# Optimization experiments

Hardware: AMD Instinct MI355X
Metric: run time of the kernel (lower is better)

## Reference

```python
import jax, jax.numpy as jnp
from jax import lax
import numpy as np

COST_CLASS, COST_BBOX, COST_GIOU = 2.0, 5.0, 2.0
ALPHA, GAMMA, OTA_K = 0.25, 2.0, 5
EXPANDED_STRIDES = 32.0
DEG = 180.0 / np.pi


def _make_corners(key, prefix):
    k1, k2, k3, k4, k5 = jax.random.split(key, 5)
    cx = jax.random.uniform(k1, prefix, minval=0.0, maxval=512.0)
    cy = jax.random.uniform(k2, prefix, minval=0.0, maxval=512.0)
    w = jax.random.uniform(k3, prefix, minval=8.0, maxval=128.0)
    h = jax.random.uniform(k4, prefix, minval=8.0, maxval=128.0)
    ang = jax.random.uniform(k5, prefix, minval=0.0, maxval=np.pi)
    offs = jnp.array([[-0.5, -0.5], [0.5, -0.5], [0.5, 0.5], [-0.5, 0.5]], jnp.float32)
    wh = jnp.stack([w, h], -1)[..., None, :]          # [..., 1, 2]
    pts = offs * wh                                    # [..., 4, 2]
    c, s = jnp.cos(ang)[..., None], jnp.sin(ang)[..., None]
    rx = pts[..., 0] * c - pts[..., 1] * s + cx[..., None]
    ry = pts[..., 0] * s + pts[..., 1] * c + cy[..., None]
    return jnp.stack([rx, ry], -1).reshape(prefix + (8,))


def setup_inputs() -> dict:
    key = jax.random.key(0)
    k1, k2, k3, k4 = jax.random.split(key, 4)
    B, Q, G, C = 16, 4096, 128, 80
    return {
        "pred_logits": jax.random.normal(k1, (B, Q, C), jnp.float32),
        "pred_boxes": _make_corners(k2, (B, Q)),
        "gt_boxes": _make_corners(k3, (B, G)),
        "gt_labels": jax.random.randint(k4, (B, G), 0, C),
    }


def corners_to_cxcywha(c):  # [N,8] -> [N,5]
    xc = (c[:, 0] + c[:, 2] + c[:, 4] + c[:, 6]) / 4
    yc = (c[:, 1] + c[:, 3] + c[:, 5] + c[:, 7]) / 4
    w = jnp.sqrt((c[:, 0] - c[:, 2]) ** 2 + (c[:, 1] - c[:, 3]) ** 2)
    h = jnp.sqrt((c[:, 2] - c[:, 4]) ** 2 + (c[:, 3] - c[:, 5]) ** 2)
    ang = jnp.arctan2(c[:, 3] - c[:, 1], c[:, 2] - c[:, 0]) * DEG
    return jnp.stack([xc, yc, w, h, ang], 1)


def _aabb(b5):
    cx, cy, w, h = b5[:, 0], b5[:, 1], b5[:, 2], b5[:, 3]
    return jnp.stack([cx - w / 2, cy - h / 2, cx + w / 2, cy + h / 2], 1)


def pairwise_iou(b1, b2):
    a, b = _aabb(b1), _aabb(b2)
    lt = jnp.maximum(a[:, None, :2], b[None, :, :2])
    rb = jnp.minimum(a[:, None, 2:], b[None, :, 2:])
    wh = jnp.clip(rb - lt, 0.0)
    inter = wh[..., 0] * wh[..., 1]
    area1 = (a[:, 2] - a[:, 0]) * (a[:, 3] - a[:, 1])
    area2 = (b[:, 2] - b[:, 0]) * (b[:, 3] - b[:, 1])
    return inter / (area1[:, None] + area2[None, :] - inter + 1e-8)


def pairwise_diou(b1, b2):
    iou = pairwise_iou(b1, b2)
    a, b = _aabb(b1), _aabb(b2)
    enc = jnp.maximum(a[:, None, 2:], b[None, :, 2:]) - jnp.minimum(a[:, None, :2], b[None, :, :2])
    c2 = (enc ** 2).sum(-1) + 1e-8
    d2 = ((b1[:, None, :2] - b2[None, :, :2]) ** 2).sum(-1)
    return iou - d2 / c2


def get_in_boxes_info(boxes, gts):
    bc = boxes.reshape(-1, 4, 2).mean(1)   # [Q,2]
    gp = gts.reshape(-1, 4, 2)             # [G,4,2]
    gc = gp.mean(1)                        # [G,2]
    cdist = jnp.sqrt(((bc[:, None] - gc[None]) ** 2).sum(-1))  # [Q,G]
    v1 = gp[:, 1] - gp[:, 0]
    v2 = gp[:, 2] - gp[:, 0]
    gt_area = jnp.abs(v1[:, 0] * v2[:, 1] - v1[:, 1] * v2[:, 0]) / 2
    diag = jnp.sqrt(((gp.max(1) - gp.min(1)) ** 2).sum(-1))
    radius = diag / EXPANDED_STRIDES
    in_boxes = cdist <= (gt_area / radius)[None, :]
    in_centers = cdist <= radius[None, :]
    return in_boxes.any(1), in_boxes & in_centers


def _dedup(cost, m):
    multi = m.sum(1) > 1
    onehot = jax.nn.one_hot(jnp.argmin(cost, 1), cost.shape[1], dtype=m.dtype)
    return jnp.where(multi[:, None], onehot, m)


def _match_single(logits, pboxes, gboxes, glabels):
    Q, G = pboxes.shape[0], gboxes.shape[0]
    prob = jax.nn.sigmoid(logits)
    fg_mask, _ = get_in_boxes_info(pboxes, gboxes)
    p5, g5 = corners_to_cxcywha(pboxes), corners_to_cxcywha(gboxes)
    ious = pairwise_iou(p5, g5)
    neg = (1 - ALPHA) * prob ** GAMMA * -jnp.log(1 - prob + 1e-8)
    pos = ALPHA * (1 - prob) ** GAMMA * -jnp.log(prob + 1e-8)
    cost_class = (pos - neg)[:, glabels]                         # [Q,G]
    cost_bbox = jnp.abs(pboxes[:, None] - gboxes[None]).sum(-1)  # L1 cdist on corners
    cost_giou = -pairwise_diou(p5, g5)
    # NB: source has `+ self.cost_giou * -cost_giou`, i.e. +w*diou; replicated verbatim.
    cost = COST_BBOX * cost_bbox + COST_CLASS * cost_class + COST_GIOU * (-cost_giou)
    cost = cost + 10000.0 * (~fg_mask)[:, None].astype(cost.dtype)
    # dynamic-k: sum of top OTA_K ious per gt, truncated to int, min 1
    topk = lax.top_k(ious.T, OTA_K)[0]                 # [G, k]
    dyn_k = jnp.clip(topk.sum(-1).astype(jnp.int32), 1, Q)
    ranks = jnp.argsort(jnp.argsort(cost, axis=0), axis=0)  # ascending-cost rank per column
    matching = (ranks < dyn_k[None, :]).astype(cost.dtype)
    matching = _dedup(cost, matching)
    # ensure every gt matched (bounded replication of the while loop)
    def cond(carry):
        c, m, it = carry
        return jnp.any(m.sum(0) == 0) & (it < G)
    def body(carry):
        c, m, it = carry
        c = c + 100000.0 * (m.sum(1) > 0)[:, None].astype(c.dtype)
        unm = m.sum(0) == 0
        amin = jnp.argmin(c, 0)                          # [G]
        hit = (jnp.arange(Q)[:, None] == amin[None, :]) & unm[None, :]
        m = jnp.where(hit, 1.0, m)
        m = _dedup(c, m)
        return (c, m, it + 1)
    _, matching, _ = lax.while_loop(cond, body, (cost, matching, jnp.int32(0)))
    return matching, cost, ious


def reference(pred_logits, pred_boxes, gt_boxes, gt_labels):
    return jax.vmap(_match_single)(pred_logits, pred_boxes, gt_boxes, gt_labels)
```

## Files before the change

### kernel.cpp

```cpp
#include <hip/hip_runtime.h>
#include <cstdint>
#include <cstddef>

#define B_ 16
#define Q_ 4096
#define G_ 128
#define C_ 80
#define QCHUNK 16
#define NCH (Q_ / QCHUNK)

typedef unsigned long long u64;
#define U64MAX 0xffffffffffffffffull

__device__ __forceinline__ u64 packkey(float v, int q) {
    unsigned int bts = __float_as_uint(v);
    if (bts == 0x80000000u) bts = 0u;
    bts = (bts & 0x80000000u) ? ~bts : (bts | 0x80000000u);
    return ((u64)bts << 32) | (unsigned int)q;
}

__device__ __forceinline__ u64 umin64(u64 a, u64 b) { return a < b ? a : b; }
__device__ __forceinline__ u64 umax64(u64 a, u64 b) { return a > b ? a : b; }

__device__ __forceinline__ void merge5_desc(
    float& a0, float& a1, float& a2, float& a3, float& a4,
    float b0, float b1, float b2, float b3, float b4)
{
    const float r0 = fmaxf(a0, b0);
    const float r1 = fmaxf(fmaxf(a1, b1), fminf(a0, b0));
    const float r2 = fmaxf(fmaxf(a2, b2), fmaxf(fminf(a0, b1), fminf(a1, b0)));
    const float r3 = fmaxf(fmaxf(a3, b3),
                     fmaxf(fminf(a0, b2), fmaxf(fminf(a1, b1), fminf(a2, b0))));
    const float r4 = fmaxf(fmaxf(a4, b4),
                     fmaxf(fmaxf(fminf(a0, b3), fminf(a3, b0)),
                           fmaxf(fminf(a1, b2), fminf(a2, b1))));
    a0 = r0; a1 = r1; a2 = r2; a3 = r3; a4 = r4;
}

__device__ __forceinline__ void merge5_asc(
    u64& a0, u64& a1, u64& a2, u64& a3, u64& a4,
    u64 b0, u64 b1, u64 b2, u64 b3, u64 b4)
{
    const u64 r0 = umin64(a0, b0);
    const u64 r1 = umin64(umin64(a1, b1), umax64(a0, b0));
    const u64 r2 = umin64(umin64(a2, b2), umin64(umax64(a0, b1), umax64(a1, b0)));
    const u64 r3 = umin64(umin64(a3, b3),
                   umin64(umax64(a0, b2), umin64(umax64(a1, b1), umax64(a2, b0))));
    const u64 r4 = umin64(umin64(a4, b4),
                   umin64(umin64(umax64(a0, b3), umax64(a3, b0)),
                          umin64(umax64(a1, b2), umax64(a2, b1))));
    a0 = r0; a1 = r1; a2 = r2; a3 = r3; a4 = r4;
}

__device__ __forceinline__ float focal_cost(float x) {
    float p;
    if (x >= 0.f) { const float e = expf(-x); p = 1.f / (1.f + e); }
    else          { const float e = expf(x);  p = e / (1.f + e); }
    const float pos = 0.25f * (1.f - p) * (1.f - p) * (-logf(p + 1e-8f));
    const float neg = 0.75f * p * p * (-logf(1.f - p + 1e-8f));
    return pos - neg;
}

__global__ __launch_bounds__(256) void fused_cost_kernel(
    const float* __restrict__ logits,
    const float* __restrict__ pboxes,
    const float* __restrict__ gboxes,
    const int*   __restrict__ glabels,
    float* __restrict__ out_cost,
    float* __restrict__ out_iou,
    float* __restrict__ costT,
    float* __restrict__ piou,
    u64*   __restrict__ pcost,
    int*   __restrict__ ramin)
{
    const int tid = threadIdx.x;
    const int g   = tid & 127;
    const int qh  = tid >> 7;
    const int ci  = blockIdx.x, b = blockIdx.y;
    const int q0  = ci * QCHUNK;

    __shared__ float pq[QCHUNK][16];
    __shared__ int   fgf[QCHUNK];
    __shared__ __align__(16) char lk_buf[5120];
    __shared__ float ctile[QCHUNK][G_ + 1];
    __shared__ float phalf[G_][5];
    float* lbuf = (float*)lk_buf;
    u64 (*khalf)[5] = (u64(*)[5])lk_buf;

    const float4* gb4 = (const float4*)(gboxes + ((size_t)b * G_ + g) * 8);
    const float4 gA = gb4[0], gB = gb4[1];
    const float g0 = gA.x, g1 = gA.y, g2 = gA.z, g3 = gA.w;
    const float g4 = gB.x, g5 = gB.y, g6 = gB.z, g7 = gB.w;
    const float gxc = (g0 + g2 + g4 + g6) * 0.25f;
    const float gyc = (g1 + g3 + g5 + g7) * 0.25f;
    const float gw = sqrtf((g0 - g2) * (g0 - g2) + (g1 - g3) * (g1 - g3));
    const float gh = sqrtf((g2 - g4) * (g2 - g4) + (g3 - g5) * (g3 - g5));
    const float gax0 = gxc - gw * 0.5f, gay0 = gyc - gh * 0.5f;
    const float gax1 = gxc + gw * 0.5f, gay1 = gyc + gh * 0.5f;
    const float garea = (gax1 - gax0) * (gay1 - gay0);
    const float v1x = g2 - g0, v1y = g3 - g1, v2x = g4 - g0, v2y = g5 - g1;
    const float gt_area = fabsf(v1x * v2y - v1y * v2x) * 0.5f;
    const float mxx = fmaxf(fmaxf(g0, g2), fmaxf(g4, g6));
    const float mnx = fminf(fminf(g0, g2), fminf(g4, g6));
    const float mxy = fmaxf(fmaxf(g1, g3), fmaxf(g5, g7));
    const float mny = fminf(fminf(g1, g3), fminf(g5, g7));
    const float dgx = mxx - mnx, dgy = mxy - mny;
    const float radius = sqrtf(dgx * dgx + dgy * dgy) / 32.0f;
    const float thresh = gt_area / radius;
    const int lab = glabels[b * G_ + g];

    if (tid < 32) {
        const float4 v = ((const float4*)(pboxes + ((size_t)b * Q_ + q0) * 8))[tid];
        *(float4*)&pq[tid >> 1][(tid & 1) * 4] = v;
    }
    __syncthreads();
    if (tid < QCHUNK) {
        const float* pr = pq[tid];
        const float p0 = pr[0], p1 = pr[1], p2 = pr[2], p3 = pr[3];
        const float p4 = pr[4], p5v = pr[5], p6 = pr[6], p7 = pr[7];
        const float pxc = (p0 + p2 + p4 + p6) * 0.25f;
        const float pyc = (p1 + p3 + p5v + p7) * 0.25f;
        const float pw = sqrtf((p0 - p2) * (p0 - p2) + (p1 - p3) * (p1 - p3));
        const float ph = sqrtf((p2 - p4) * (p2 - p4) + (p3 - p5v) * (p3 - p5v));
        pq[tid][8]  = pxc;
        pq[tid][9]  = pyc;
        pq[tid][10] = pxc - pw * 0.5f;
        pq[tid][11] = pyc - ph * 0.5f;
        pq[tid][12] = pxc + pw * 0.5f;
        pq[tid][13] = pyc + ph * 0.5f;
        pq[tid][14] = pw * ph;
        fgf[tid] = 0;
    }
    __syncthreads();
    for (int j = tid; j < QCHUNK * 80; j += 256)
        lbuf[j] = focal_cost(logits[((size_t)b * Q_ + q0) * 80 + j]);

    const int lane0 = ((tid & 63) == 0);
    for (int i = 0; i < QCHUNK / 2; ++i) {
        const int ql = 2 * i + qh;
        const float dx = pq[ql][8] - gxc, dy = pq[ql][9] - gyc;
        const int in = sqrtf(dx * dx + dy * dy) <= thresh;
        const int anyin = __any(in);
        if (anyin && lane0) fgf[ql] = 1;
    }
    __syncthreads();

    float t0 = -1e38f, t1 = -1e38f, t2 = -1e38f, t3 = -1e38f, t4 = -1e38f;
    u64 k0 = U64MAX, k1 = U64MAX, k2 = U64MAX, k3 = U64MAX, k4 = U64MAX;

    #pragma unroll
    for (int jj = 0; jj < 8; ++jj) {
        const int qls = 2 * jj + qh;
        const int q   = q0 + qls;
        const float4 prA = *(const float4*)&pq[qls][0];
        const float4 prB = *(const float4*)&pq[qls][4];
        const float4 prC = *(const float4*)&pq[qls][8];
        const float4 prD = *(const float4*)&pq[qls][12];
        const float p0 = prA.x, p1 = prA.y, p2 = prA.z, p3 = prA.w;
        const float p4 = prB.x, p5v = prB.y, p6 = prB.z, p7 = prB.w;
        const float pxc = prC.x, pyc = prC.y;
        const float pax0 = prC.z, pay0 = prC.w, pax1 = prD.x, pay1 = prD.y;
        const float parea = prD.z;

        const float l1 = fabsf(p0 - g0) + fabsf(p1 - g1) + fabsf(p2 - g2)
                       + fabsf(p3 - g3) + fabsf(p4 - g4) + fabsf(p5v - g5)
                       + fabsf(p6 - g6) + fabsf(p7 - g7);

        const float ltx = fmaxf(pax0, gax0), lty = fmaxf(pay0, gay0);
        const float rbx = fminf(pax1, gax1), rby = fminf(pay1, gay1);
        const float iw = fmaxf(rbx - ltx, 0.f), ih = fmaxf(rby - lty, 0.f);
        const float inter = iw * ih;
        const float iou = inter / (parea + garea - inter + 1e-8f);

        const float ew = fmaxf(pax1, gax1) - fminf(pax0, gax0);
        const float eh = fmaxf(pay1, gay1) - fminf(pay0, gay0);
        const float cc2 = ew * ew + eh * eh + 1e-8f;
        const float dx = pxc - gxc, dy = pyc - gyc;
        const float diou = iou - (dx * dx + dy * dy) / cc2;

        const float cclass = lbuf[qls * 80 + lab];
        const float cost = 5.f * l1 + 2.f * cclass + 2.f * diou
                         + (fgf[qls] ? 0.f : 10000.f);

        const size_t o = ((size_t)b * Q_ + q) * G_ + g;
        out_cost[o] = cost;
        out_iou[o]  = iou;
        ctile[qls][g] = cost;

        if (iou > t4) {
            if (iou > t0)      { t4 = t3; t3 = t2; t2 = t1; t1 = t0; t0 = iou; }
            else if (iou > t1) { t4 = t3; t3 = t2; t2 = t1; t1 = iou; }
            else if (iou > t2) { t4 = t3; t3 = t2; t2 = iou; }
            else if (iou > t3) { t4 = t3; t3 = iou; }
            else               { t4 = iou; }
        }
        const u64 kk = packkey(cost, q);
        if (kk < k4) {
            if (kk < k0)      { k4 = k3; k3 = k2; k2 = k1; k1 = k0; k0 = kk; }
            else if (kk < k1) { k4 = k3; k3 = k2; k2 = k1; k1 = kk; }
            else if (kk < k2) { k4 = k3; k3 = k2; k2 = kk; }
            else if (kk < k3) { k4 = k3; k3 = kk; }
            else              { k4 = kk; }
        }
    }
    __syncthreads();

    for (int t = tid; t < QCHUNK * G_ / 4; t += 256) {
        const int gg = t >> 2;
        const int k  = (t & 3) << 2;
        float4 o;
        o.x = ctile[k + 0][gg]; o.y = ctile[k + 1][gg];
        o.z = ctile[k + 2][gg]; o.w = ctile[k + 3][gg];
        *(float4*)&costT[((size_t)b * G_ + gg) * Q_ + q0 + k] = o;
    }

    {
        const int qls  = tid >> 4;
        const int part = tid & 15;
        float v = 1e38f; int mg = 0x7fffffff;
        #pragma unroll
        for (int j = 0; j < 8; ++j) {
            const int gg = part + 16 * j;
            const float c = ctile[qls][gg];
            if (c < v || (c == v && gg < mg)) { v = c; mg = gg; }
        }
        #pragma unroll
        for (int off = 1; off < 16; off <<= 1) {
            const float ov = __shfl_xor(v, off);
            const int   og = __shfl_xor(mg, off);
            if (ov < v || (ov == v && og < mg)) { v = ov; mg = og; }
        }
        if (part == 0) ramin[b * Q_ + q0 + qls] = mg;
    }

    if (qh == 1) {
        phalf[g][0] = t0; phalf[g][1] = t1; phalf[g][2] = t2;
        phalf[g][3] = t3; phalf[g][4] = t4;
        khalf[g][0] = k0; khalf[g][1] = k1; khalf[g][2] = k2;
        khalf[g][3] = k3; khalf[g][4] = k4;
    }
    __syncthreads();
    if (qh == 0) {
        merge5_desc(t0, t1, t2, t3, t4,
                    phalf[g][0], phalf[g][1], phalf[g][2], phalf[g][3], phalf[g][4]);
        merge5_asc(k0, k1, k2, k3, k4,
                   khalf[g][0], khalf[g][1], khalf[g][2], khalf[g][3], khalf[g][4]);
        const size_t pbase = (((size_t)b * G_ + g) * NCH + ci) * 5;
        piou[pbase + 0] = t0; piou[pbase + 1] = t1; piou[pbase + 2] = t2;
        piou[pbase + 3] = t3; piou[pbase + 4] = t4;
        pcost[pbase + 0] = k0; pcost[pbase + 1] = k1; pcost[pbase + 2] = k2;
        pcost[pbase + 3] = k3; pcost[pbase + 4] = k4;
    }
}

__global__ __launch_bounds__(256) void dynk_scatter_kernel(
    const u64*   __restrict__ pcost,
    const float* __restrict__ piou,
    u64* __restrict__ cand,
    int* __restrict__ cnt,
    int* __restrict__ gsel)
{
    const int col = blockIdx.x;
    const int b = col >> 7, g = col & 127;
    const int tid = threadIdx.x;
    const int wv = tid >> 6, ln = tid & 63;

    __shared__ u64   wl[4][5];
    __shared__ float il[4][5];

    const size_t base = (size_t)col * (NCH * 5) + (size_t)tid * 5;

    u64 k0 = pcost[base + 0], k1 = pcost[base + 1], k2 = pcost[base + 2],
        k3 = pcost[base + 3], k4 = pcost[base + 4];
    float t0 = piou[base + 0], t1 = piou[base + 1], t2 = piou[base + 2],
          t3 = piou[base + 3], t4 = piou[base + 4];

    #pragma unroll
    for (int off = 1; off < 64; off <<= 1) {
        merge5_asc(k0, k1, k2, k3, k4,
                   __shfl_xor(k0, off), __shfl_xor(k1, off), __shfl_xor(k2, off),
                   __shfl_xor(k3, off), __shfl_xor(k4, off));
        merge5_desc(t0, t1, t2, t3, t4,
                    __shfl_xor(t0, off), __shfl_xor(t1, off), __shfl_xor(t2, off),
                    __shfl_xor(t3, off), __shfl_xor(t4, off));
    }
    if (ln == 0) {
        wl[wv][0] = k0; wl[wv][1] = k1; wl[wv][2] = k2; wl[wv][3] = k3; wl[wv][4] = k4;
        il[wv][0] = t0; il[wv][1] = t1; il[wv][2] = t2; il[wv][3] = t3; il[wv][4] = t4;
    }
    __syncthreads();

    if (tid == 0) {
        u64 f0 = wl[0][0], f1 = wl[0][1], f2 = wl[0][2], f3 = wl[0][3], f4 = wl[0][4];
        merge5_asc(f0, f1, f2, f3, f4, wl[1][0], wl[1][1], wl[1][2], wl[1][3], wl[1][4]);
        merge5_asc(f0, f1, f2, f3, f4, wl[2][0], wl[2][1], wl[2][2], wl[2][3], wl[2][4]);
        merge5_asc(f0, f1, f2, f3, f4, wl[3][0], wl[3][1], wl[3][2], wl[3][3], wl[3][4]);
        float s0 = il[0][0], s1 = il[0][1], s2 = il[0][2], s3 = il[0][3], s4 = il[0][4];
        merge5_desc(s0, s1, s2, s3, s4, il[1][0], il[1][1], il[1][2], il[1][3], il[1][4]);
        merge5_desc(s0, s1, s2, s3, s4, il[2][0], il[2][1], il[2][2], il[2][3], il[2][4]);
        merge5_desc(s0, s1, s2, s3, s4, il[3][0], il[3][1], il[3][2], il[3][3], il[3][4]);

        cand[(size_t)col * 5 + 0] = f0;
        cand[(size_t)col * 5 + 1] = f1;
        cand[(size_t)col * 5 + 2] = f2;
        cand[(size_t)col * 5 + 3] = f3;
        cand[(size_t)col * 5 + 4] = f4;

        const float s = s0 + s1 + s2 + s3 + s4;
        int dynk = (int)s;
        if (dynk < 1) dynk = 1;
        if (dynk > 5) dynk = 5;
        const u64 ks[5] = {f0, f1, f2, f3, f4};
        #pragma unroll
        for (int i = 0; i < 5; ++i) {
            if (i < dynk) {
                const int q = (int)(ks[i] & 0xffffffffu);
                atomicAdd(&cnt[b * Q_ + q], 1);
                gsel[b * Q_ + q] = g;
            }
        }
    }
}

__global__ __launch_bounds__(256) void loop_kernel(
    const float* __restrict__ costT,
    const int* __restrict__ cnt,
    const int* __restrict__ gsel,
    const int* __restrict__ ramin,
    const u64* __restrict__ cand,
    int* __restrict__ rmatch_final)
{
    const int b = blockIdx.x, tid = threadIdx.x;
    const int wv = tid >> 6, ln = tid & 63;

    __shared__ short rmatch[Q_];
    __shared__ unsigned char s_ra[Q_];
    __shared__ int newh[Q_];
    __shared__ unsigned char newg[Q_];
    __shared__ u64 scand[G_][5];
    __shared__ int ptrs[G_], col_cnt[G_], unm_list[G_], prop[G_], fb_slot[G_], touched[G_];
    __shared__ int n_unm, n_fb, n_touch;

    for (int q = tid; q < Q_; q += 256) {
        const int c  = cnt[b * Q_ + q];
        const int ra = ramin[b * Q_ + q];
        s_ra[q] = (unsigned char)ra;
        newh[q] = 0;
        rmatch[q] = (c == 0) ? (short)-1
                             : (c == 1 ? (short)gsel[b * Q_ + q] : (short)ra);
    }
    if (tid < G_) { col_cnt[tid] = 0; ptrs[tid] = 0; }
    for (int i = tid; i < G_ * 5; i += 256)
        scand[i / 5][i % 5] = cand[(size_t)b * G_ * 5 + i];
    __syncthreads();
    for (int q = tid; q < Q_; q += 256)
        if (rmatch[q] >= 0) atomicAdd(&col_cnt[rmatch[q]], 1);
    __syncthreads();

    for (int it = 0; it < G_; ++it) {
        if (tid == 0) { n_unm = 0; n_fb = 0; n_touch = 0; }
        __syncthreads();
        if (tid < G_ && col_cnt[tid] == 0)
            unm_list[atomicAdd(&n_unm, 1)] = tid;
        __syncthreads();
        const int nu = n_unm;
        if (nu == 0) break;

        if (tid < nu) {
            const int g = unm_list[tid];
            int p = ptrs[g];
            int q = -1;
            while (p < 5) {
                const int cq = (int)(scand[g][p] & 0xffffffffu);
                if (rmatch[cq] < 0) { q = cq; break; }
                ++p;
            }
            ptrs[g] = p;
            prop[tid] = q;
            if (q < 0) fb_slot[atomicAdd(&n_fb, 1)] = tid;
        }
        __syncthreads();

        const int nf = n_fb;
        for (int i = wv; i < nf; i += 4) {
            const int slot = fb_slot[i];
            const int g = unm_list[slot];
            const float4* colp = (const float4*)(costT + ((size_t)b * G_ + g) * Q_);
            u64 k0 = U64MAX, k1 = U64MAX, k2 = U64MAX, k3 = U64MAX, k4 = U64MAX;
            #pragma unroll 4
            for (int s = 0; s < Q_ / 256; ++s) {
                const int idx = ln + s * 64;
                const float4 c4 = colp[idx];
                const int qb = idx * 4;
                const float vv[4] = {c4.x, c4.y, c4.z, c4.w};
                #pragma unroll
                for (int j = 0; j < 4; ++j) {
                    if (rmatch[qb + j] < 0) {
                        const u64 kk = packkey(vv[j], qb + j);
                        if (kk < k4) {
                            if (kk < k0)      { k4 = k3; k3 = k2; k2 = k1; k1 = k0; k0 = kk; }
                            else if (kk < k1) { k4 = k3; k3 = k2; k2 = k1; k1 = kk; }
                            else if (kk < k2) { k4 = k3; k3 = k2; k2 = kk; }
                            else if (kk < k3) { k4 = k3; k3 = kk; }
                            else              { k4 = kk; }
                        }
                    }
                }
            }
            #pragma unroll
            for (int off = 1; off < 64; off <<= 1) {
                merge5_asc(k0, k1, k2, k3, k4,
                           __shfl_xor(k0, off), __shfl_xor(k1, off), __shfl_xor(k2, off),
                           __shfl_xor(k3, off), __shfl_xor(k4, off));
            }
            if (ln == 0) {
                scand[g][0] = k0; scand[g][1] = k1; scand[g][2] = k2;
                scand[g][3] = k3; scand[g][4] = k4;
                ptrs[g] = 0;
                prop[slot] = (int)(k0 & 0xffffffffu);
            }
        }
        __syncthreads();

        if (tid < nu) {
            const int q = prop[tid];
            newg[q] = (unsigned char)unm_list[tid];
            if (atomicAdd(&newh[q], 1) == 0)
                touched[atomicAdd(&n_touch, 1)] = q;
        }
        __syncthreads();

        const int nt = n_touch;
        if (tid < nt) {
            const int q = touched[tid];
            const int nh = newh[q];
            const int gg = (nh == 1) ? (int)newg[q] : (int)s_ra[q];
            rmatch[q] = (short)gg;
            atomicAdd(&col_cnt[gg], 1);
            newh[q] = 0;
        }
        __syncthreads();
    }

    for (int q = tid; q < Q_; q += 256)
        rmatch_final[b * Q_ + q] = rmatch[q];
}

__global__ __launch_bounds__(256) void expand_kernel(
    const int* __restrict__ rmatch_final, float* __restrict__ out_match)
{
    const int idx = blockIdx.x * 256 + threadIdx.x;
    const int row = idx >> 5;
    const int gb  = (idx & 31) << 2;
    const int rm  = rmatch_final[row];
    float4 o;
    o.x = (rm == gb)     ? 1.f : 0.f;
    o.y = (rm == gb + 1) ? 1.f : 0.f;
    o.z = (rm == gb + 2) ? 1.f : 0.f;
    o.w = (rm == gb + 3) ? 1.f : 0.f;
    ((float4*)out_match)[idx] = o;
}

extern "C" void kernel_launch(void* const* d_in, const int* in_sizes, int n_in,
                              void* d_out, int out_size, void* d_ws, size_t ws_size,
                              hipStream_t stream) {
    const float* logits  = (const float*)d_in[0];
    const float* pboxes  = (const float*)d_in[1];
    const float* gboxes  = (const float*)d_in[2];
    const int*   glabels = (const int*)d_in[3];

    float* out = (float*)d_out;
    const size_t BQG = (size_t)B_ * Q_ * G_;
    float* out_match = out;
    float* out_cost  = out + BQG;
    float* out_iou   = out + 2 * BQG;

    char* ws = (char*)d_ws;
    size_t off = 0;
    float* costT  = (float*)(ws + off); off += (size_t)B_ * G_ * Q_ * 4;
    u64*   pcost  = (u64*)  (ws + off); off += (size_t)B_ * G_ * NCH * 5 * 8;
    float* piou   = (float*)(ws + off); off += (size_t)B_ * G_ * NCH * 5 * 4;
    u64*   cand   = (u64*)  (ws + off); off += (size_t)B_ * G_ * 5 * 8;
    int*   ramin  = (int*)  (ws + off); off += (size_t)B_ * Q_ * 4;
    int*   cnt    = (int*)  (ws + off); off += (size_t)B_ * Q_ * 4;
    int*   gsel   = (int*)  (ws + off); off += (size_t)B_ * Q_ * 4;
    int*   rmf    = (int*)  (ws + off); off += (size_t)B_ * Q_ * 4;

    hipMemsetAsync(cnt, 0, (size_t)B_ * Q_ * 4, stream);
    fused_cost_kernel<<<dim3(NCH, B_), 256, 0, stream>>>(
        logits, pboxes, gboxes, glabels, out_cost, out_iou, costT, piou, pcost, ramin);
    dynk_scatter_kernel<<<B_ * G_, 256, 0, stream>>>(pcost, piou, cand, cnt, gsel);
    loop_kernel<<<B_, 256, 0, stream>>>(costT, cnt, gsel, ramin, cand, rmf);
    expand_kernel<<<(int)(BQG / 4 / 256), 256, 0, stream>>>(rmf, out_match);
}
```

Before: 201.4 us.

## Use branchless top-5 inserts, transpose partial layout, widen loop kernel to 1024 threads

Replaces the branchy top-5 insertion with branchless min/max insertion networks, split into two independent chains that are merged at the end to add instruction-level parallelism. Changes the partial top-k layout so the cost kernel writes contiguously across g and the scatter kernel reads with the new indexing. Uses pointer increments for the output stores. Raises the serial loop_kernel from 256 to 1024 threads per block, so 16 waves scan fallback columns instead of 4, at the price of more per-block synchronisation.

```diff
diff --git a/kernel.cpp b/kernel.cpp
--- a/kernel.cpp
+++ b/kernel.cpp
@@ -21,6 +21,24 @@
 
 __device__ __forceinline__ u64 umin64(u64 a, u64 b) { return a < b ? a : b; }
 __device__ __forceinline__ u64 umax64(u64 a, u64 b) { return a > b ? a : b; }
+
+__device__ __forceinline__ void ins5_asc(u64& k0, u64& k1, u64& k2, u64& k3, u64& k4, u64 c) {
+    u64 n;
+    n = umin64(k0, c); c = umax64(k0, c); k0 = n;
+    n = umin64(k1, c); c = umax64(k1, c); k1 = n;
+    n = umin64(k2, c); c = umax64(k2, c); k2 = n;
+    n = umin64(k3, c); c = umax64(k3, c); k3 = n;
+    k4 = umin64(k4, c);
+}
+
+__device__ __forceinline__ void ins5_desc(float& t0, float& t1, float& t2, float& t3, float& t4, float c) {
+    float n;
+    n = fmaxf(t0, c); c = fminf(t0, c); t0 = n;
+    n = fmaxf(t1, c); c = fminf(t1, c); t1 = n;
+    n = fmaxf(t2, c); c = fminf(t2, c); t2 = n;
+    n = fmaxf(t3, c); c = fminf(t3, c); t3 = n;
+    t4 = fmaxf(t4, c);
+}
 
 __device__ __forceinline__ void merge5_desc(
     float& a0, float& a1, float& a2, float& a3, float& a4,
@@ -145,8 +163,13 @@
     }
     __syncthreads();
 
-    float t0 = -1e38f, t1 = -1e38f, t2 = -1e38f, t3 = -1e38f, t4 = -1e38f;
-    u64 k0 = U64MAX, k1 = U64MAX, k2 = U64MAX, k3 = U64MAX, k4 = U64MAX;
+    float ta0 = -1e38f, ta1 = -1e38f, ta2 = -1e38f, ta3 = -1e38f, ta4 = -1e38f;
+    float tb0 = -1e38f, tb1 = -1e38f, tb2 = -1e38f, tb3 = -1e38f, tb4 = -1e38f;
+    u64 ka0 = U64MAX, ka1 = U64MAX, ka2 = U64MAX, ka3 = U64MAX, ka4 = U64MAX;
+    u64 kb0 = U64MAX, kb1 = U64MAX, kb2 = U64MAX, kb3 = U64MAX, kb4 = U64MAX;
+
+    float* pc = out_cost + ((size_t)b * Q_ + q0 + qh) * G_ + g;
+    float* pi = out_iou  + ((size_t)b * Q_ + q0 + qh) * G_ + g;
 
     #pragma unroll
     for (int jj = 0; jj < 8; ++jj) {
@@ -182,27 +205,22 @@
         const float cost = 5.f * l1 + 2.f * cclass + 2.f * diou
                          + (fgf[qls] ? 0.f : 10000.f);
 
-        const size_t o = ((size_t)b * Q_ + q) * G_ + g;
-        out_cost[o] = cost;
-        out_iou[o]  = iou;
+        *pc = cost; pc += 2 * G_;
+        *pi = iou;  pi += 2 * G_;
         ctile[qls][g] = cost;
 
-        if (iou > t4) {
-            if (iou > t0)      { t4 = t3; t3 = t2; t2 = t1; t1 = t0; t0 = iou; }
-            else if (iou > t1) { t4 = t3; t3 = t2; t2 = t1; t1 = iou; }
-            else if (iou > t2) { t4 = t3; t3 = t2; t2 = iou; }
-            else if (iou > t3) { t4 = t3; t3 = iou; }
-            else               { t4 = iou; }
-        }
         const u64 kk = packkey(cost, q);
-        if (kk < k4) {
-            if (kk < k0)      { k4 = k3; k3 = k2; k2 = k1; k1 = k0; k0 = kk; }
-            else if (kk < k1) { k4 = k3; k3 = k2; k2 = k1; k1 = kk; }
-            else if (kk < k2) { k4 = k3; k3 = k2; k2 = kk; }
-            else if (kk < k3) { k4 = k3; k3 = kk; }
-            else              { k4 = kk; }
-        }
-    }
+        if (jj < 4) {
+            ins5_desc(ta0, ta1, ta2, ta3, ta4, iou);
+            ins5_asc(ka0, ka1, ka2, ka3, ka4, kk);
+        } else {
+            ins5_desc(tb0, tb1, tb2, tb3, tb4, iou);
+            ins5_asc(kb0, kb1, kb2, kb3, kb4, kk);
+        }
+    }
+    merge5_desc(ta0, ta1, ta2, ta3, ta4, tb0, tb1, tb2, tb3, tb4);
+    merge5_asc(ka0, ka1, ka2, ka3, ka4, kb0, kb1, kb2, kb3, kb4);
+
     __syncthreads();
 
     for (int t = tid; t < QCHUNK * G_ / 4; t += 256) {
@@ -234,22 +252,22 @@
     }
 
     if (qh == 1) {
-        phalf[g][0] = t0; phalf[g][1] = t1; phalf[g][2] = t2;
-        phalf[g][3] = t3; phalf[g][4] = t4;
-        khalf[g][0] = k0; khalf[g][1] = k1; khalf[g][2] = k2;
-        khalf[g][3] = k3; khalf[g][4] = k4;
+        phalf[g][0] = ta0; phalf[g][1] = ta1; phalf[g][2] = ta2;
+        phalf[g][3] = ta3; phalf[g][4] = ta4;
+        khalf[g][0] = ka0; khalf[g][1] = ka1; khalf[g][2] = ka2;
+        khalf[g][3] = ka3; khalf[g][4] = ka4;
     }
     __syncthreads();
     if (qh == 0) {
-        merge5_desc(t0, t1, t2, t3, t4,
+        merge5_desc(ta0, ta1, ta2, ta3, ta4,
                     phalf[g][0], phalf[g][1], phalf[g][2], phalf[g][3], phalf[g][4]);
-        merge5_asc(k0, k1, k2, k3, k4,
+        merge5_asc(ka0, ka1, ka2, ka3, ka4,
                    khalf[g][0], khalf[g][1], khalf[g][2], khalf[g][3], khalf[g][4]);
-        const size_t pbase = (((size_t)b * G_ + g) * NCH + ci) * 5;
-        piou[pbase + 0] = t0; piou[pbase + 1] = t1; piou[pbase + 2] = t2;
-        piou[pbase + 3] = t3; piou[pbase + 4] = t4;
-        pcost[pbase + 0] = k0; pcost[pbase + 1] = k1; pcost[pbase + 2] = k2;
-        pcost[pbase + 3] = k3; pcost[pbase + 4] = k4;
+        const size_t pbase = (((size_t)b * NCH + ci) * G_ + g) * 5;
+        piou[pbase + 0] = ta0; piou[pbase + 1] = ta1; piou[pbase + 2] = ta2;
+        piou[pbase + 3] = ta3; piou[pbase + 4] = ta4;
+        pcost[pbase + 0] = ka0; pcost[pbase + 1] = ka1; pcost[pbase + 2] = ka2;
+        pcost[pbase + 3] = ka3; pcost[pbase + 4] = ka4;
     }
 }
 
@@ -268,7 +286,7 @@
     __shared__ u64   wl[4][5];
     __shared__ float il[4][5];
 
-    const size_t base = (size_t)col * (NCH * 5) + (size_t)tid * 5;
+    const size_t base = (((size_t)b * NCH + tid) * G_ + g) * 5;
 
     u64 k0 = pcost[base + 0], k1 = pcost[base + 1], k2 = pcost[base + 2],
         k3 = pcost[base + 3], k4 = pcost[base + 4];
@@ -322,7 +340,7 @@
     }
 }
 
-__global__ __launch_bounds__(256) void loop_kernel(
+__global__ __launch_bounds__(1024) void loop_kernel(
     const float* __restrict__ costT,
     const int* __restrict__ cnt,
     const int* __restrict__ gsel,
@@ -341,7 +359,7 @@
     __shared__ int ptrs[G_], col_cnt[G_], unm_list[G_], prop[G_], fb_slot[G_], touched[G_];
     __shared__ int n_unm, n_fb, n_touch;
 
-    for (int q = tid; q < Q_; q += 256) {
+    for (int q = tid; q < Q_; q += 1024) {
         const int c  = cnt[b * Q_ + q];
         const int ra = ramin[b * Q_ + q];
         s_ra[q] = (unsigned char)ra;
@@ -350,10 +368,10 @@
                              : (c == 1 ? (short)gsel[b * Q_ + q] : (short)ra);
     }
     if (tid < G_) { col_cnt[tid] = 0; ptrs[tid] = 0; }
-    for (int i = tid; i < G_ * 5; i += 256)
-        scand[i / 5][i % 5] = cand[(size_t)b * G_ * 5 + i];
-    __syncthreads();
-    for (int q = tid; q < Q_; q += 256)
+    if (tid < G_ * 5)
+        scand[tid / 5][tid % 5] = cand[(size_t)b * G_ * 5 + tid];
+    __syncthreads();
+    for (int q = tid; q < Q_; q += 1024)
         if (rmatch[q] >= 0) atomicAdd(&col_cnt[rmatch[q]], 1);
     __syncthreads();
 
@@ -382,7 +400,7 @@
         __syncthreads();
 
         const int nf = n_fb;
-        for (int i = wv; i < nf; i += 4) {
+        for (int i = wv; i < nf; i += 16) {
             const int slot = fb_slot[i];
             const int g = unm_list[slot];
             const float4* colp = (const float4*)(costT + ((size_t)b * G_ + g) * Q_);
@@ -395,16 +413,8 @@
                 const float vv[4] = {c4.x, c4.y, c4.z, c4.w};
                 #pragma unroll
                 for (int j = 0; j < 4; ++j) {
-                    if (rmatch[qb + j] < 0) {
-                        const u64 kk = packkey(vv[j], qb + j);
-                        if (kk < k4) {
-                            if (kk < k0)      { k4 = k3; k3 = k2; k2 = k1; k1 = k0; k0 = kk; }
-                            else if (kk < k1) { k4 = k3; k3 = k2; k2 = k1; k1 = kk; }
-                            else if (kk < k2) { k4 = k3; k3 = k2; k2 = kk; }
-                            else if (kk < k3) { k4 = k3; k3 = kk; }
-                            else              { k4 = kk; }
-                        }
-                    }
+                    if (rmatch[qb + j] < 0)
+                        ins5_asc(k0, k1, k2, k3, k4, packkey(vv[j], qb + j));
                 }
             }
             #pragma unroll
@@ -442,7 +452,7 @@
         __syncthreads();
     }
 
-    for (int q = tid; q < Q_; q += 256)
+    for (int q = tid; q < Q_; q += 1024)
         rmatch_final[b * Q_ + q] = rmatch[q];
 }
 
@@ -490,6 +500,6 @@
     fused_cost_kernel<<<dim3(NCH, B_), 256, 0, stream>>>(
         logits, pboxes, gboxes, glabels, out_cost, out_iou, costT, piou, pcost, ramin);
     dynk_scatter_kernel<<<B_ * G_, 256, 0, stream>>>(pcost, piou, cand, cnt, gsel);
-    loop_kernel<<<B_, 256, 0, stream>>>(costT, cnt, gsel, ramin, cand, rmf);
+    loop_kernel<<<B_, 1024, 0, stream>>>(costT, cnt, gsel, ramin, cand, rmf);
     expand_kernel<<<(int)(BQG / 4 / 256), 256, 0, stream>>>(rmf, out_match);
 }
```

After: 215.4 us. 7.0% more time.
